# Kernel tuning notes

Measured on AMD Instinct MI355X. Metric: run time of the kernel, lower is better.

Reference implementation:

```python
import jax, jax.numpy as jnp
import numpy as np

FFT_BINS = 513   # win_length//2 + 1
WIN = 1024       # win_length
H = 128          # LSTM hidden size (both blocks)
ENC = 256        # encoder_size
EPS = 1e-7


def _lstm_cell(x, h, c, Wih, Whh, bih, bhh):
    # x: [1, in], h/c: [1, H]; PyTorch gate order i, f, g, o
    g = x @ Wih.T + bih + h @ Whh.T + bhh
    i, f, gg, o = jnp.split(g, 4, axis=-1)
    c2 = jax.nn.sigmoid(f) * c + jax.nn.sigmoid(i) * jnp.tanh(gg)
    h2 = jax.nn.sigmoid(o) * jnp.tanh(c2)
    return h2, c2


def _sep_block(x, states, Wih0, Whh0, bih0, bhh0, Wih1, Whh1, bih1, bhh1, dw, db):
    # x: [1,1,in]; states: [1,1,2*2*H] -> [2(h/c), 2(layers), 1, H]
    st = states.reshape(2, 2, 1, H)
    h0, c0 = st[0], st[1]
    xt = x[:, 0]                                   # [1, in]
    h1, c1 = _lstm_cell(xt, h0[0], c0[0], Wih0, Whh0, bih0, bhh0)
    h2, c2 = _lstm_cell(h1, h0[1], c0[1], Wih1, Whh1, bih1, bhh1)
    mask = jax.nn.sigmoid(h2 @ dw.T + db)[:, None, :]   # [1,1,in]
    out_states = jnp.stack([jnp.stack([h1, h2]), jnp.stack([c1, c2])]).reshape(1, 1, -1)
    return mask, out_states


def setup_inputs() -> dict:
    key = jax.random.key(0)
    ks = jax.random.split(key, 32)
    s = 0.08  # ~ 1/sqrt(H), matching PyTorch LSTM init scale
    def n(i, shape, sc=s):
        return jax.random.normal(ks[i], shape, dtype=jnp.float32) * sc
    inp = {
        "mag": jax.random.uniform(ks[0], (1, 1, FFT_BINS), dtype=jnp.float32),
        "phase": n(1, (1, 1, FFT_BINS), 3.0),
        "in_states1": n(2, (1, 1, 2 * 2 * H), 1.0),
        "in_states2": n(3, (1, 1, 2 * 2 * H), 1.0),
        # sep1 LSTM (input 513)
        "w_ih1_0": n(4, (4 * H, FFT_BINS)), "w_hh1_0": n(5, (4 * H, H)),
        "b_ih1_0": n(6, (4 * H,)), "b_hh1_0": n(7, (4 * H,)),
        "w_ih1_1": n(8, (4 * H, H)), "w_hh1_1": n(9, (4 * H, H)),
        "b_ih1_1": n(10, (4 * H,)), "b_hh1_1": n(11, (4 * H,)),
        "dense1_w": n(12, (FFT_BINS, H)), "dense1_b": n(13, (FFT_BINS,)),
        # encoder 1x1 conv (no bias) + instant layernorm
        "enc_w": n(14, (ENC, WIN)),
        "gamma": jnp.ones((1, 1, ENC), jnp.float32),
        "beta": jnp.zeros((1, 1, ENC), jnp.float32),
        # sep2 LSTM (input 256)
        "w_ih2_0": n(15, (4 * H, ENC)), "w_hh2_0": n(16, (4 * H, H)),
        "b_ih2_0": n(17, (4 * H,)), "b_hh2_0": n(18, (4 * H,)),
        "w_ih2_1": n(19, (4 * H, H)), "w_hh2_1": n(20, (4 * H, H)),
        "b_ih2_1": n(21, (4 * H,)), "b_hh2_1": n(22, (4 * H,)),
        "dense2_w": n(23, (ENC, H)), "dense2_b": n(24, (ENC,)),
        # decoder 1x1 conv (no bias)
        "dec_w": n(25, (WIN, ENC)),
    }
    return inp


def reference(mag, phase, in_states1, in_states2,
              w_ih1_0, w_hh1_0, b_ih1_0, b_hh1_0,
              w_ih1_1, w_hh1_1, b_ih1_1, b_hh1_1,
              dense1_w, dense1_b, enc_w, gamma, beta,
              w_ih2_0, w_hh2_0, b_ih2_0, b_hh2_0,
              w_ih2_1, w_hh2_1, b_ih2_1, b_hh2_1,
              dense2_w, dense2_b, dec_w):
    # Branch 1: magnitude masking in STFT domain
    mask1, out_states1 = _sep_block(mag, in_states1, w_ih1_0, w_hh1_0, b_ih1_0,
                                    b_hh1_0, w_ih1_1, w_hh1_1, b_ih1_1, b_hh1_1,
                                    dense1_w, dense1_b)
    est_mag = mask1 * mag
    s1_stft = est_mag * jnp.exp(1j * phase)          # [1,1,513] complex64
    y1 = jnp.fft.irfft(s1_stft, axis=-1)             # [1,1,1024]
    # encoder 1x1 conv (permute + conv1d(k=1) == matmul over channels)
    enc = jnp.einsum('btw,ew->bte', y1, enc_w)       # [1,1,256]
    # instant layer norm over channels
    mean = jnp.mean(enc, axis=-1, keepdims=True)
    var = jnp.mean(jnp.square(enc - mean), axis=-1, keepdims=True)
    enc_norm = (enc - mean) / jnp.sqrt(var + EPS) * gamma + beta
    # Branch 2: learned-domain masking
    mask2, out_states2 = _sep_block(enc_norm, in_states2, w_ih2_0, w_hh2_0,
                                    b_ih2_0, b_hh2_0, w_ih2_1, w_hh2_1,
                                    b_ih2_1, b_hh2_1, dense2_w, dense2_b)
    est_enc = mask2 * enc
    decoded = jnp.einsum('bte,we->bwt', est_enc, dec_w)  # [1,1024,1]
    return decoded, out_states1, out_states2
```

## Files before the change

kernel.cpp:

```cpp
#include <hip/hip_runtime.h>
#include <hip/hip_bf16.h>


#define HDIM 128
typedef __hip_bfloat16 bf16;

__device__ float G[4608];
#define O_H1A 0
#define O_H2A 128
#define O_C1A 256
#define O_C2A 384
#define O_H1B 512
#define O_H2B 640
#define O_C1B 768
#define O_C2B 896
#define O_XR  1024
#define O_XI  1600
#define O_Y   2176
#define O_ENC 3200
#define O_EST 3456

__device__ __forceinline__ bool is_bf(const void* probe) {
    return (((const unsigned*)probe)[0] & 0xFFFFu) == 0x3F80u;
}
__device__ __forceinline__ float ldin(const void* p, int i, bool bf) {
    return bf ? __bfloat162float(((const bf16*)p)[i]) : ((const float*)p)[i];
}
__device__ __forceinline__ void stout(void* p, int i, float v, bool bf) {
    if (bf) ((bf16*)p)[i] = __float2bfloat16(v);
    else    ((float*)p)[i] = v;
}
__device__ __forceinline__ float wred(float v) {
#pragma unroll
    for (int m = 32; m; m >>= 1) v += __shfl_xor(v, m);
    return v;
}
__device__ __forceinline__ float sigm(float x) { return 1.f / (1.f + expf(-x)); }

template <int LX, bool XINT>
__global__ __launch_bounds__(256) void k_lstm(
    const void* __restrict__ xp, int xoff,
    const void* __restrict__ st, int hoff, int coff,
    const void* __restrict__ Wih, const void* __restrict__ Whh,
    const void* __restrict__ bih, const void* __restrict__ bhh,
    int ho, int co, const void* __restrict__ probe)
{
    const bool bf = is_bf(probe);
    __shared__ float xs[LX];
    __shared__ float hs[HDIM];
    __shared__ float g4[4];
    const int tid = threadIdx.x, lane = tid & 63, wave = tid >> 6;
    const int j = blockIdx.x;
    for (int i = tid; i < LX; i += 256)
        xs[i] = XINT ? G[xoff + i] : ldin(xp, xoff + i, bf);
    for (int i = tid; i < HDIM; i += 256)
        hs[i] = ldin(st, hoff + i, bf);
    __syncthreads();
    const int row = wave * HDIM + j;
    float acc = 0.f;
    for (int k = lane; k < LX; k += 64) acc += ldin(Wih, row * LX + k, bf) * xs[k];
    for (int k = lane; k < HDIM; k += 64) acc += ldin(Whh, row * HDIM + k, bf) * hs[k];
    acc = wred(acc);
    if (lane == 0) g4[wave] = acc + ldin(bih, row, bf) + ldin(bhh, row, bf);
    __syncthreads();
    if (tid == 0) {
        float cin = ldin(st, coff + j, bf);
        float c2 = sigm(g4[1]) * cin + sigm(g4[0]) * tanhf(g4[2]);
        float h2 = sigm(g4[3]) * tanhf(c2);
        G[ho + j] = h2;
        G[co + j] = c2;
    }
}

__global__ __launch_bounds__(256) void k_lstm_ln(
    const void* __restrict__ gamma, const void* __restrict__ beta,
    const void* __restrict__ st,
    const void* __restrict__ Wih, const void* __restrict__ Whh,
    const void* __restrict__ bih, const void* __restrict__ bhh,
    const void* __restrict__ probe)
{
    const bool bf = is_bf(probe);
    __shared__ float xs[256];
    __shared__ float hs[HDIM];
    __shared__ float red[4];
    __shared__ float g4[4];
    const int tid = threadIdx.x, lane = tid & 63, wave = tid >> 6;
    const int j = blockIdx.x;
    float v = G[O_ENC + tid];
    float s = wred(v);
    if (lane == 0) red[wave] = s;
    __syncthreads();
    float mean = (red[0] + red[1] + red[2] + red[3]) * (1.f / 256.f);
    __syncthreads();
    float d = v - mean;
    float s2 = wred(d * d);
    if (lane == 0) red[wave] = s2;
    __syncthreads();
    float var = (red[0] + red[1] + red[2] + red[3]) * (1.f / 256.f);
    float rs = rsqrtf(var + 1e-7f);
    xs[tid] = d * rs * ldin(gamma, tid, bf) + ldin(beta, tid, bf);
    for (int i = tid; i < HDIM; i += 256) hs[i] = ldin(st, i, bf);
    __syncthreads();
    const int row = wave * HDIM + j;
    float acc = 0.f;
    for (int k = lane; k < 256; k += 64) acc += ldin(Wih, row * 256 + k, bf) * xs[k];
    for (int k = lane; k < HDIM; k += 64) acc += ldin(Whh, row * HDIM + k, bf) * hs[k];
    acc = wred(acc);
    if (lane == 0) g4[wave] = acc + ldin(bih, row, bf) + ldin(bhh, row, bf);
    __syncthreads();
    if (tid == 0) {
        float cin = ldin(st, 256 + j, bf);
        float c2 = sigm(g4[1]) * cin + sigm(g4[0]) * tanhf(g4[2]);
        float h2 = sigm(g4[3]) * tanhf(c2);
        G[O_H1B + j] = h2;
        G[O_C1B + j] = c2;
    }
}

__global__ __launch_bounds__(256) void k_mask1(
    const void* __restrict__ dw, const void* __restrict__ db,
    const void* __restrict__ mag, const void* __restrict__ phase,
    void* __restrict__ out, const void* __restrict__ probe)
{
    const bool bf = is_bf(probe);
    __shared__ float hs[HDIM];
    const int tid = threadIdx.x, lane = tid & 63, wave = tid >> 6;
    for (int i = tid; i < HDIM; i += 256) hs[i] = G[O_H2A + i];
    __syncthreads();
    const int g = blockIdx.x * 4 + wave;
    if (g < 513) {
        float acc = 0.f;
        for (int k = lane; k < HDIM; k += 64) acc += ldin(dw, g * HDIM + k, bf) * hs[k];
        acc = wred(acc);
        if (lane == 0) {
            float m = sigm(acc + ldin(db, g, bf));
            float em = m * ldin(mag, g, bf);
            float p = ldin(phase, g, bf);
            float sp, cp;
            sincosf(p, &sp, &cp);
            G[O_XR + g] = em * cp;
            G[O_XI + g] = em * sp;
        }
    }
    if (blockIdx.x == 0) {
        for (int t = tid; t < 512; t += 256) stout(out, 1024 + t, G[t], bf);
    }
}

__global__ __launch_bounds__(256) void k_irfft()
{
    __shared__ float xr[513], xi[513];
    const int tid = threadIdx.x, lane = tid & 63, wave = tid >> 6;
    for (int i = tid; i < 513; i += 256) { xr[i] = G[O_XR + i]; xi[i] = G[O_XI + i]; }
    __syncthreads();
    const int n = blockIdx.x * 4 + wave;
    float acc = 0.f;
    for (int k = lane; k < 513; k += 64) {
        if (k == 0) {
            acc += xr[0];
        } else if (k == 512) {
            acc += (n & 1) ? -xr[512] : xr[512];
        } else {
            int m = (k * n) & 1023;
            float th = (float)m * (6.283185307179586f / 1024.f);
            float sn, cs;
            sincosf(th, &sn, &cs);
            acc += 2.f * (xr[k] * cs - xi[k] * sn);
        }
    }
    acc = wred(acc);
    if (lane == 0) G[O_Y + n] = acc * (1.f / 1024.f);
}

__global__ __launch_bounds__(256) void k_enc(
    const void* __restrict__ ew, const void* __restrict__ probe)
{
    const bool bf = is_bf(probe);
    __shared__ float ys[1024];
    const int tid = threadIdx.x, lane = tid & 63, wave = tid >> 6;
    for (int i = tid; i < 1024; i += 256) ys[i] = G[O_Y + i];
    __syncthreads();
    const int e = blockIdx.x * 4 + wave;
    float acc = 0.f;
    for (int k = lane; k < 1024; k += 64) acc += ldin(ew, e * 1024 + k, bf) * ys[k];
    acc = wred(acc);
    if (lane == 0) G[O_ENC + e] = acc;
}

__global__ __launch_bounds__(256) void k_mask2(
    const void* __restrict__ dw, const void* __restrict__ db,
    void* __restrict__ out, const void* __restrict__ probe)
{
    const bool bf = is_bf(probe);
    __shared__ float hs[HDIM];
    const int tid = threadIdx.x, lane = tid & 63, wave = tid >> 6;
    for (int i = tid; i < HDIM; i += 256) hs[i] = G[O_H2B + i];
    __syncthreads();
    const int e = blockIdx.x * 4 + wave;
    float acc = 0.f;
    for (int k = lane; k < HDIM; k += 64) acc += ldin(dw, e * HDIM + k, bf) * hs[k];
    acc = wred(acc);
    if (lane == 0) {
        float m = sigm(acc + ldin(db, e, bf));
        G[O_EST + e] = m * G[O_ENC + e];
    }
    if (blockIdx.x == 0) {
        for (int t = tid; t < 512; t += 256) stout(out, 1536 + t, G[512 + t], bf);
    }
}

__global__ __launch_bounds__(256) void k_dec(
    const void* __restrict__ dw, void* __restrict__ out, const void* __restrict__ probe)
{
    const bool bf = is_bf(probe);
    __shared__ float es[256];
    const int tid = threadIdx.x, lane = tid & 63, wave = tid >> 6;
    es[tid] = G[O_EST + tid];
    __syncthreads();
    const int w = blockIdx.x * 4 + wave;
    float acc = 0.f;
    for (int k = lane; k < 256; k += 64) acc += ldin(dw, w * 256 + k, bf) * es[k];
    acc = wred(acc);
    if (lane == 0) stout(out, w, acc, bf);
}

extern "C" void kernel_launch(void* const* d_in, const int* in_sizes, int n_in,
                              void* d_out, int out_size, void* d_ws, size_t ws_size,
                              hipStream_t stream)
{
    const void* mag      = d_in[0];
    const void* phase    = d_in[1];
    const void* st1      = d_in[2];
    const void* st2      = d_in[3];
    const void* w_ih1_0  = d_in[4];
    const void* w_hh1_0  = d_in[5];
    const void* b_ih1_0  = d_in[6];
    const void* b_hh1_0  = d_in[7];
    const void* w_ih1_1  = d_in[8];
    const void* w_hh1_1  = d_in[9];
    const void* b_ih1_1  = d_in[10];
    const void* b_hh1_1  = d_in[11];
    const void* dense1_w = d_in[12];
    const void* dense1_b = d_in[13];
    const void* enc_w    = d_in[14];
    const void* gamma    = d_in[15];
    const void* beta     = d_in[16];
    const void* w_ih2_0  = d_in[17];
    const void* w_hh2_0  = d_in[18];
    const void* b_ih2_0  = d_in[19];
    const void* b_hh2_0  = d_in[20];
    const void* w_ih2_1  = d_in[21];
    const void* w_hh2_1  = d_in[22];
    const void* b_ih2_1  = d_in[23];
    const void* b_hh2_1  = d_in[24];
    const void* dense2_w = d_in[25];
    const void* dense2_b = d_in[26];
    const void* dec_w    = d_in[27];

    k_lstm<513, false><<<128, 256, 0, stream>>>(
        mag, 0, st1, 0, 256, w_ih1_0, w_hh1_0, b_ih1_0, b_hh1_0, O_H1A, O_C1A, gamma);
    k_lstm<128, true><<<128, 256, 0, stream>>>(
        nullptr, O_H1A, st1, 128, 384, w_ih1_1, w_hh1_1, b_ih1_1, b_hh1_1, O_H2A, O_C2A, gamma);
    k_mask1<<<129, 256, 0, stream>>>(dense1_w, dense1_b, mag, phase, d_out, gamma);

    k_irfft<<<256, 256, 0, stream>>>();
    k_enc<<<64, 256, 0, stream>>>(enc_w, gamma);

    k_lstm_ln<<<128, 256, 0, stream>>>(
        gamma, beta, st2, w_ih2_0, w_hh2_0, b_ih2_0, b_hh2_0, gamma);
    k_lstm<128, true><<<128, 256, 0, stream>>>(
        nullptr, O_H1B, st2, 128, 384, w_ih2_1, w_hh2_1, b_ih2_1, b_hh2_1, O_H2B, O_C2B, gamma);
    k_mask2<<<64, 256, 0, stream>>>(dense2_w, dense2_b, d_out, gamma);

    k_dec<<<256, 256, 0, stream>>>(dec_w, d_out, gamma);
}
```

Baseline: 152.8 us.

## Fuse all stages into one cooperative kernel with grid syncs and twiddle table

Replaces nine separate kernel launches with a single cooperative kernel of 128 blocks that runs the stages in sequence, separated by grid-wide syncs. The goal is to remove per-launch overhead and inter-kernel gaps in this latency-bound, single-timestep pipeline. The inverse FFT now reads a shared-memory cos/sin table instead of calling sincosf per term. In exchange, parallelism drops to 128 blocks for the irfft, encoder and decoder stages, and each grid sync adds its own barrier latency.

Result: slower. 288.5 us (+88.8%).

```diff
diff --git a/kernel.cpp b/kernel.cpp
--- a/kernel.cpp
+++ b/kernel.cpp
@@ -1,5 +1,8 @@
 #include <hip/hip_runtime.h>
 #include <hip/hip_bf16.h>
+#include <hip/hip_cooperative_groups.h>
+
+namespace cg = cooperative_groups;
 
 
 #define HDIM 128
@@ -37,240 +40,223 @@
 }
 __device__ __forceinline__ float sigm(float x) { return 1.f / (1.f + expf(-x)); }
 
-template <int LX, bool XINT>
-__global__ __launch_bounds__(256) void k_lstm(
-    const void* __restrict__ xp, int xoff,
-    const void* __restrict__ st, int hoff, int coff,
-    const void* __restrict__ Wih, const void* __restrict__ Whh,
-    const void* __restrict__ bih, const void* __restrict__ bhh,
-    int ho, int co, const void* __restrict__ probe)
+struct Params {
+    const void *mag, *phase, *st1, *st2;
+    const void *wih10, *whh10, *bih10, *bhh10;
+    const void *wih11, *whh11, *bih11, *bhh11;
+    const void *d1w, *d1b, *encw, *gamma, *beta;
+    const void *wih20, *whh20, *bih20, *bhh20;
+    const void *wih21, *whh21, *bih21, *bhh21;
+    const void *d2w, *d2b, *decw;
+    void *out;
+};
+
+__global__ __launch_bounds__(256, 1) void k_fused(Params p)
 {
-    const bool bf = is_bf(probe);
-    __shared__ float xs[LX];
+    cg::grid_group gg = cg::this_grid();
+    const bool bf = is_bf(p.gamma);
+    const int tid  = threadIdx.x, lane = tid & 63, wave = tid >> 6;
+    const int b    = blockIdx.x;
+    const int wgid = b * 4 + wave;
+
+    __shared__ float tc[1024], ts[1024];
+    __shared__ float xbuf[1024];
+    __shared__ float xib[513];
     __shared__ float hs[HDIM];
     __shared__ float g4[4];
-    const int tid = threadIdx.x, lane = tid & 63, wave = tid >> 6;
-    const int j = blockIdx.x;
-    for (int i = tid; i < LX; i += 256)
-        xs[i] = XINT ? G[xoff + i] : ldin(xp, xoff + i, bf);
-    for (int i = tid; i < HDIM; i += 256)
-        hs[i] = ldin(st, hoff + i, bf);
-    __syncthreads();
-    const int row = wave * HDIM + j;
-    float acc = 0.f;
-    for (int k = lane; k < LX; k += 64) acc += ldin(Wih, row * LX + k, bf) * xs[k];
-    for (int k = lane; k < HDIM; k += 64) acc += ldin(Whh, row * HDIM + k, bf) * hs[k];
-    acc = wred(acc);
-    if (lane == 0) g4[wave] = acc + ldin(bih, row, bf) + ldin(bhh, row, bf);
+    __shared__ float red[4];
+
+    for (int i = tid; i < 1024; i += 256) {
+        float th = (float)i * (6.283185307179586f / 1024.f);
+        sincosf(th, &ts[i], &tc[i]);
+    }
+
+    for (int i = tid; i < 513; i += 256) xbuf[i] = ldin(p.mag, i, bf);
+    for (int i = tid; i < HDIM; i += 256) hs[i] = ldin(p.st1, i, bf);
+    __syncthreads();
+    {
+        const int row = wave * HDIM + b;
+        float acc = 0.f;
+        for (int k = lane; k < 513; k += 64) acc += ldin(p.wih10, row * 513 + k, bf) * xbuf[k];
+        for (int k = lane; k < HDIM; k += 64) acc += ldin(p.whh10, row * HDIM + k, bf) * hs[k];
+        acc = wred(acc);
+        if (lane == 0) g4[wave] = acc + ldin(p.bih10, row, bf) + ldin(p.bhh10, row, bf);
+    }
     __syncthreads();
     if (tid == 0) {
-        float cin = ldin(st, coff + j, bf);
+        float cin = ldin(p.st1, 256 + b, bf);
         float c2 = sigm(g4[1]) * cin + sigm(g4[0]) * tanhf(g4[2]);
-        float h2 = sigm(g4[3]) * tanhf(c2);
-        G[ho + j] = h2;
-        G[co + j] = c2;
-    }
-}
-
-__global__ __launch_bounds__(256) void k_lstm_ln(
-    const void* __restrict__ gamma, const void* __restrict__ beta,
-    const void* __restrict__ st,
-    const void* __restrict__ Wih, const void* __restrict__ Whh,
-    const void* __restrict__ bih, const void* __restrict__ bhh,
-    const void* __restrict__ probe)
-{
-    const bool bf = is_bf(probe);
-    __shared__ float xs[256];
-    __shared__ float hs[HDIM];
-    __shared__ float red[4];
-    __shared__ float g4[4];
-    const int tid = threadIdx.x, lane = tid & 63, wave = tid >> 6;
-    const int j = blockIdx.x;
-    float v = G[O_ENC + tid];
-    float s = wred(v);
-    if (lane == 0) red[wave] = s;
-    __syncthreads();
-    float mean = (red[0] + red[1] + red[2] + red[3]) * (1.f / 256.f);
-    __syncthreads();
-    float d = v - mean;
-    float s2 = wred(d * d);
-    if (lane == 0) red[wave] = s2;
-    __syncthreads();
-    float var = (red[0] + red[1] + red[2] + red[3]) * (1.f / 256.f);
-    float rs = rsqrtf(var + 1e-7f);
-    xs[tid] = d * rs * ldin(gamma, tid, bf) + ldin(beta, tid, bf);
-    for (int i = tid; i < HDIM; i += 256) hs[i] = ldin(st, i, bf);
-    __syncthreads();
-    const int row = wave * HDIM + j;
-    float acc = 0.f;
-    for (int k = lane; k < 256; k += 64) acc += ldin(Wih, row * 256 + k, bf) * xs[k];
-    for (int k = lane; k < HDIM; k += 64) acc += ldin(Whh, row * HDIM + k, bf) * hs[k];
-    acc = wred(acc);
-    if (lane == 0) g4[wave] = acc + ldin(bih, row, bf) + ldin(bhh, row, bf);
+        G[O_H1A + b] = sigm(g4[3]) * tanhf(c2);
+        G[O_C1A + b] = c2;
+    }
+    gg.sync();
+
+    for (int i = tid; i < HDIM; i += 256) { xbuf[i] = G[O_H1A + i]; hs[i] = ldin(p.st1, 128 + i, bf); }
+    __syncthreads();
+    {
+        const int row = wave * HDIM + b;
+        float acc = 0.f;
+        for (int k = lane; k < HDIM; k += 64) acc += ldin(p.wih11, row * HDIM + k, bf) * xbuf[k];
+        for (int k = lane; k < HDIM; k += 64) acc += ldin(p.whh11, row * HDIM + k, bf) * hs[k];
+        acc = wred(acc);
+        if (lane == 0) g4[wave] = acc + ldin(p.bih11, row, bf) + ldin(p.bhh11, row, bf);
+    }
     __syncthreads();
     if (tid == 0) {
-        float cin = ldin(st, 256 + j, bf);
+        float cin = ldin(p.st1, 384 + b, bf);
         float c2 = sigm(g4[1]) * cin + sigm(g4[0]) * tanhf(g4[2]);
-        float h2 = sigm(g4[3]) * tanhf(c2);
-        G[O_H1B + j] = h2;
-        G[O_C1B + j] = c2;
-    }
-}
-
-__global__ __launch_bounds__(256) void k_mask1(
-    const void* __restrict__ dw, const void* __restrict__ db,
-    const void* __restrict__ mag, const void* __restrict__ phase,
-    void* __restrict__ out, const void* __restrict__ probe)
-{
-    const bool bf = is_bf(probe);
-    __shared__ float hs[HDIM];
-    const int tid = threadIdx.x, lane = tid & 63, wave = tid >> 6;
+        G[O_H2A + b] = sigm(g4[3]) * tanhf(c2);
+        G[O_C2A + b] = c2;
+    }
+    gg.sync();
+
     for (int i = tid; i < HDIM; i += 256) hs[i] = G[O_H2A + i];
     __syncthreads();
-    const int g = blockIdx.x * 4 + wave;
-    if (g < 513) {
-        float acc = 0.f;
-        for (int k = lane; k < HDIM; k += 64) acc += ldin(dw, g * HDIM + k, bf) * hs[k];
+    for (int g = wgid; g < 513; g += 512) {
+        float acc = 0.f;
+        for (int k = lane; k < HDIM; k += 64) acc += ldin(p.d1w, g * HDIM + k, bf) * hs[k];
         acc = wred(acc);
         if (lane == 0) {
-            float m = sigm(acc + ldin(db, g, bf));
-            float em = m * ldin(mag, g, bf);
-            float p = ldin(phase, g, bf);
+            float m = sigm(acc + ldin(p.d1b, g, bf));
+            float em = m * ldin(p.mag, g, bf);
+            float ph = ldin(p.phase, g, bf);
             float sp, cp;
-            sincosf(p, &sp, &cp);
+            sincosf(ph, &sp, &cp);
             G[O_XR + g] = em * cp;
             G[O_XI + g] = em * sp;
         }
     }
-    if (blockIdx.x == 0) {
-        for (int t = tid; t < 512; t += 256) stout(out, 1024 + t, G[t], bf);
-    }
-}
-
-__global__ __launch_bounds__(256) void k_irfft()
-{
-    __shared__ float xr[513], xi[513];
-    const int tid = threadIdx.x, lane = tid & 63, wave = tid >> 6;
-    for (int i = tid; i < 513; i += 256) { xr[i] = G[O_XR + i]; xi[i] = G[O_XI + i]; }
-    __syncthreads();
-    const int n = blockIdx.x * 4 + wave;
-    float acc = 0.f;
-    for (int k = lane; k < 513; k += 64) {
-        if (k == 0) {
-            acc += xr[0];
-        } else if (k == 512) {
-            acc += (n & 1) ? -xr[512] : xr[512];
-        } else {
-            int m = (k * n) & 1023;
-            float th = (float)m * (6.283185307179586f / 1024.f);
-            float sn, cs;
-            sincosf(th, &sn, &cs);
-            acc += 2.f * (xr[k] * cs - xi[k] * sn);
-        }
-    }
-    acc = wred(acc);
-    if (lane == 0) G[O_Y + n] = acc * (1.f / 1024.f);
-}
-
-__global__ __launch_bounds__(256) void k_enc(
-    const void* __restrict__ ew, const void* __restrict__ probe)
-{
-    const bool bf = is_bf(probe);
-    __shared__ float ys[1024];
-    const int tid = threadIdx.x, lane = tid & 63, wave = tid >> 6;
-    for (int i = tid; i < 1024; i += 256) ys[i] = G[O_Y + i];
-    __syncthreads();
-    const int e = blockIdx.x * 4 + wave;
-    float acc = 0.f;
-    for (int k = lane; k < 1024; k += 64) acc += ldin(ew, e * 1024 + k, bf) * ys[k];
-    acc = wred(acc);
-    if (lane == 0) G[O_ENC + e] = acc;
-}
-
-__global__ __launch_bounds__(256) void k_mask2(
-    const void* __restrict__ dw, const void* __restrict__ db,
-    void* __restrict__ out, const void* __restrict__ probe)
-{
-    const bool bf = is_bf(probe);
-    __shared__ float hs[HDIM];
-    const int tid = threadIdx.x, lane = tid & 63, wave = tid >> 6;
+    if (b == 0) {
+        for (int t = tid; t < 512; t += 256) stout(p.out, 1024 + t, G[t], bf);
+    }
+    gg.sync();
+
+    for (int i = tid; i < 513; i += 256) { xbuf[i] = G[O_XR + i]; xib[i] = G[O_XI + i]; }
+    __syncthreads();
+#pragma unroll
+    for (int r = 0; r < 2; ++r) {
+        const int n = wgid + r * 512;
+        float acc = 0.f;
+        for (int k = lane; k < 513; k += 64) {
+            if (k == 0) {
+                acc += xbuf[0];
+            } else if (k == 512) {
+                acc += (n & 1) ? -xbuf[512] : xbuf[512];
+            } else {
+                int m = (k * n) & 1023;
+                acc += 2.f * (xbuf[k] * tc[m] - xib[k] * ts[m]);
+            }
+        }
+        acc = wred(acc);
+        if (lane == 0) G[O_Y + n] = acc * (1.f / 1024.f);
+    }
+    gg.sync();
+
+    for (int i = tid; i < 1024; i += 256) xbuf[i] = G[O_Y + i];
+    __syncthreads();
+    if (wgid < 256) {
+        float acc = 0.f;
+        for (int k = lane; k < 1024; k += 64) acc += ldin(p.encw, wgid * 1024 + k, bf) * xbuf[k];
+        acc = wred(acc);
+        if (lane == 0) G[O_ENC + wgid] = acc;
+    }
+    gg.sync();
+
+    {
+        float v = G[O_ENC + tid];
+        float s = wred(v);
+        if (lane == 0) red[wave] = s;
+        __syncthreads();
+        float mean = (red[0] + red[1] + red[2] + red[3]) * (1.f / 256.f);
+        __syncthreads();
+        float d = v - mean;
+        float s2 = wred(d * d);
+        if (lane == 0) red[wave] = s2;
+        __syncthreads();
+        float var = (red[0] + red[1] + red[2] + red[3]) * (1.f / 256.f);
+        float rs = rsqrtf(var + 1e-7f);
+        xbuf[tid] = d * rs * ldin(p.gamma, tid, bf) + ldin(p.beta, tid, bf);
+        for (int i = tid; i < HDIM; i += 256) hs[i] = ldin(p.st2, i, bf);
+        __syncthreads();
+        const int row = wave * HDIM + b;
+        float acc = 0.f;
+        for (int k = lane; k < 256; k += 64) acc += ldin(p.wih20, row * 256 + k, bf) * xbuf[k];
+        for (int k = lane; k < HDIM; k += 64) acc += ldin(p.whh20, row * HDIM + k, bf) * hs[k];
+        acc = wred(acc);
+        if (lane == 0) g4[wave] = acc + ldin(p.bih20, row, bf) + ldin(p.bhh20, row, bf);
+        __syncthreads();
+        if (tid == 0) {
+            float cin = ldin(p.st2, 256 + b, bf);
+            float c2 = sigm(g4[1]) * cin + sigm(g4[0]) * tanhf(g4[2]);
+            G[O_H1B + b] = sigm(g4[3]) * tanhf(c2);
+            G[O_C1B + b] = c2;
+        }
+    }
+    gg.sync();
+
+    for (int i = tid; i < HDIM; i += 256) { xbuf[i] = G[O_H1B + i]; hs[i] = ldin(p.st2, 128 + i, bf); }
+    __syncthreads();
+    {
+        const int row = wave * HDIM + b;
+        float acc = 0.f;
+        for (int k = lane; k < HDIM; k += 64) acc += ldin(p.wih21, row * HDIM + k, bf) * xbuf[k];
+        for (int k = lane; k < HDIM; k += 64) acc += ldin(p.whh21, row * HDIM + k, bf) * hs[k];
+        acc = wred(acc);
+        if (lane == 0) g4[wave] = acc + ldin(p.bih21, row, bf) + ldin(p.bhh21, row, bf);
+    }
+    __syncthreads();
+    if (tid == 0) {
+        float cin = ldin(p.st2, 384 + b, bf);
+        float c2 = sigm(g4[1]) * cin + sigm(g4[0]) * tanhf(g4[2]);
+        G[O_H2B + b] = sigm(g4[3]) * tanhf(c2);
+        G[O_C2B + b] = c2;
+    }
+    gg.sync();
+
     for (int i = tid; i < HDIM; i += 256) hs[i] = G[O_H2B + i];
     __syncthreads();
-    const int e = blockIdx.x * 4 + wave;
-    float acc = 0.f;
-    for (int k = lane; k < HDIM; k += 64) acc += ldin(dw, e * HDIM + k, bf) * hs[k];
-    acc = wred(acc);
-    if (lane == 0) {
-        float m = sigm(acc + ldin(db, e, bf));
-        G[O_EST + e] = m * G[O_ENC + e];
-    }
-    if (blockIdx.x == 0) {
-        for (int t = tid; t < 512; t += 256) stout(out, 1536 + t, G[512 + t], bf);
-    }
-}
-
-__global__ __launch_bounds__(256) void k_dec(
-    const void* __restrict__ dw, void* __restrict__ out, const void* __restrict__ probe)
-{
-    const bool bf = is_bf(probe);
-    __shared__ float es[256];
-    const int tid = threadIdx.x, lane = tid & 63, wave = tid >> 6;
-    es[tid] = G[O_EST + tid];
-    __syncthreads();
-    const int w = blockIdx.x * 4 + wave;
-    float acc = 0.f;
-    for (int k = lane; k < 256; k += 64) acc += ldin(dw, w * 256 + k, bf) * es[k];
-    acc = wred(acc);
-    if (lane == 0) stout(out, w, acc, bf);
+    if (wgid < 256) {
+        float acc = 0.f;
+        for (int k = lane; k < HDIM; k += 64) acc += ldin(p.d2w, wgid * HDIM + k, bf) * hs[k];
+        acc = wred(acc);
+        if (lane == 0) {
+            float m = sigm(acc + ldin(p.d2b, wgid, bf));
+            G[O_EST + wgid] = m * G[O_ENC + wgid];
+        }
+    }
+    if (b == 0) {
+        for (int t = tid; t < 512; t += 256) stout(p.out, 1536 + t, G[512 + t], bf);
+    }
+    gg.sync();
+
+    if (tid < 256) xbuf[tid] = G[O_EST + tid];
+    __syncthreads();
+#pragma unroll
+    for (int r = 0; r < 2; ++r) {
+        const int w = wgid + r * 512;
+        float acc = 0.f;
+        for (int k = lane; k < 256; k += 64) acc += ldin(p.decw, w * 256 + k, bf) * xbuf[k];
+        acc = wred(acc);
+        if (lane == 0) stout(p.out, w, acc, bf);
+    }
 }
 
 extern "C" void kernel_launch(void* const* d_in, const int* in_sizes, int n_in,
                               void* d_out, int out_size, void* d_ws, size_t ws_size,
                               hipStream_t stream)
 {
-    const void* mag      = d_in[0];
-    const void* phase    = d_in[1];
-    const void* st1      = d_in[2];
-    const void* st2      = d_in[3];
-    const void* w_ih1_0  = d_in[4];
-    const void* w_hh1_0  = d_in[5];
-    const void* b_ih1_0  = d_in[6];
-    const void* b_hh1_0  = d_in[7];
-    const void* w_ih1_1  = d_in[8];
-    const void* w_hh1_1  = d_in[9];
-    const void* b_ih1_1  = d_in[10];
-    const void* b_hh1_1  = d_in[11];
-    const void* dense1_w = d_in[12];
-    const void* dense1_b = d_in[13];
-    const void* enc_w    = d_in[14];
-    const void* gamma    = d_in[15];
-    const void* beta     = d_in[16];
-    const void* w_ih2_0  = d_in[17];
-    const void* w_hh2_0  = d_in[18];
-    const void* b_ih2_0  = d_in[19];
-    const void* b_hh2_0  = d_in[20];
-    const void* w_ih2_1  = d_in[21];
-    const void* w_hh2_1  = d_in[22];
-    const void* b_ih2_1  = d_in[23];
-    const void* b_hh2_1  = d_in[24];
-    const void* dense2_w = d_in[25];
-    const void* dense2_b = d_in[26];
-    const void* dec_w    = d_in[27];
-
-    k_lstm<513, false><<<128, 256, 0, stream>>>(
-        mag, 0, st1, 0, 256, w_ih1_0, w_hh1_0, b_ih1_0, b_hh1_0, O_H1A, O_C1A, gamma);
-    k_lstm<128, true><<<128, 256, 0, stream>>>(
-        nullptr, O_H1A, st1, 128, 384, w_ih1_1, w_hh1_1, b_ih1_1, b_hh1_1, O_H2A, O_C2A, gamma);
-    k_mask1<<<129, 256, 0, stream>>>(dense1_w, dense1_b, mag, phase, d_out, gamma);
-
-    k_irfft<<<256, 256, 0, stream>>>();
-    k_enc<<<64, 256, 0, stream>>>(enc_w, gamma);
-
-    k_lstm_ln<<<128, 256, 0, stream>>>(
-        gamma, beta, st2, w_ih2_0, w_hh2_0, b_ih2_0, b_hh2_0, gamma);
-    k_lstm<128, true><<<128, 256, 0, stream>>>(
-        nullptr, O_H1B, st2, 128, 384, w_ih2_1, w_hh2_1, b_ih2_1, b_hh2_1, O_H2B, O_C2B, gamma);
-    k_mask2<<<64, 256, 0, stream>>>(dense2_w, dense2_b, d_out, gamma);
-
-    k_dec<<<256, 256, 0, stream>>>(dec_w, d_out, gamma);
-}
+    Params hp;
+    hp.mag   = d_in[0];  hp.phase = d_in[1];  hp.st1 = d_in[2];  hp.st2 = d_in[3];
+    hp.wih10 = d_in[4];  hp.whh10 = d_in[5];  hp.bih10 = d_in[6];  hp.bhh10 = d_in[7];
+    hp.wih11 = d_in[8];  hp.whh11 = d_in[9];  hp.bih11 = d_in[10]; hp.bhh11 = d_in[11];
+    hp.d1w   = d_in[12]; hp.d1b   = d_in[13]; hp.encw  = d_in[14];
+    hp.gamma = d_in[15]; hp.beta  = d_in[16];
+    hp.wih20 = d_in[17]; hp.whh20 = d_in[18]; hp.bih20 = d_in[19]; hp.bhh20 = d_in[20];
+    hp.wih21 = d_in[21]; hp.whh21 = d_in[22]; hp.bih21 = d_in[23]; hp.bhh21 = d_in[24];
+    hp.d2w   = d_in[25]; hp.d2b   = d_in[26]; hp.decw  = d_in[27];
+    hp.out   = d_out;
+
+    void* args[] = { &hp };
+    hipLaunchCooperativeKernel((const void*)k_fused, dim3(128), dim3(256),
+                               args, 0, stream);
+}
```
